# Performance work log

Hardware: AMD Instinct MI355X
Metric: run time of the kernel (lower is better)

Reference implementation:

```python
import jax, jax.numpy as jnp
import numpy as np

V, E, H, TAGS = 50000, 128, 128, 8  # H = hidden per direction (hidden_dim // 2)
B, T = 64, 512


def _lstm_dir(x, w_ih, w_hh, b_ih, b_hh, reverse):
    # x: [B,T,I] -> hs: [B,T,H]; PyTorch gate order i,f,g,o
    xg = jnp.einsum('bti,gi->btg', x, w_ih) + b_ih + b_hh  # [B,T,4H]
    if reverse:
        xg = xg[:, ::-1]
    Bn = x.shape[0]
    Hn = w_hh.shape[1]

    def step(carry, g):
        h, c = carry
        g = g + h @ w_hh.T
        i, f, gg, o = jnp.split(g, 4, axis=-1)
        c = jax.nn.sigmoid(f) * c + jax.nn.sigmoid(i) * jnp.tanh(gg)
        h = jax.nn.sigmoid(o) * jnp.tanh(c)
        return (h, c), h

    h0 = jnp.zeros((Bn, Hn), x.dtype)
    _, hs = jax.lax.scan(step, (h0, h0), jnp.swapaxes(xg, 0, 1))
    hs = jnp.swapaxes(hs, 0, 1)
    return hs[:, ::-1] if reverse else hs


def _crf_partition(emissions, transitions):
    # emissions: [B,T,K]; scan the forward algorithm over time
    fv0 = emissions[:, 0]  # [B,K]

    def step(fv, emit):
        fv = jax.nn.logsumexp(fv[:, :, None] + transitions[None] + emit[:, None, :], axis=1)
        return fv, None

    fv, _ = jax.lax.scan(step, fv0, jnp.swapaxes(emissions[:, 1:], 0, 1))
    return jax.nn.logsumexp(fv, axis=1)  # [B]


def _forward_nll(sentences, tags, embedding, lstm_params, h2t_w, h2t_b, transitions):
    x = embedding[sentences]  # [B,T,E]; dropout inactive (eval)
    for pf, pb in lstm_params:
        x = jnp.concatenate([_lstm_dir(x, *pf, False), _lstm_dir(x, *pb, True)], axis=-1)
    emissions = x @ h2t_w.T + h2t_b  # [B,T,K]
    # gold path score (mask = all ones)
    emit_score = jnp.take_along_axis(emissions, tags[:, :, None], axis=2)[..., 0].sum(axis=1)
    trans_score = transitions[tags[:, :-1], tags[:, 1:]].sum(axis=1)
    partition = _crf_partition(emissions, transitions)
    return -(emit_score + trans_score - partition).mean()


def setup_inputs() -> dict:
    key = jax.random.key(0)
    ks = jax.random.split(key, 40)
    sc = 0.05
    inp = {}
    inp['sentences'] = jax.random.randint(ks[0], (B, T), 0, V)
    inp['tags'] = jax.random.randint(ks[1], (B, T), 0, TAGS)
    emb = jax.random.normal(ks[2], (V, E), jnp.float32) * sc
    inp['embedding'] = emb.at[0].set(0.0)  # padding_idx=0
    idx = 3
    for l in range(2):
        in_dim = E if l == 0 else 2 * H
        for d in ('', '_rev'):
            inp[f'w_ih_l{l}{d}'] = jax.random.normal(ks[idx], (4 * H, in_dim), jnp.float32) * sc; idx += 1
            inp[f'w_hh_l{l}{d}'] = jax.random.normal(ks[idx], (4 * H, H), jnp.float32) * sc; idx += 1
            inp[f'b_ih_l{l}{d}'] = jax.random.normal(ks[idx], (4 * H,), jnp.float32) * sc; idx += 1
            inp[f'b_hh_l{l}{d}'] = jax.random.normal(ks[idx], (4 * H,), jnp.float32) * sc; idx += 1
    inp['h2t_w'] = jax.random.normal(ks[idx], (TAGS, 2 * H), jnp.float32) * sc; idx += 1
    inp['h2t_b'] = jax.random.normal(ks[idx], (TAGS,), jnp.float32) * sc; idx += 1
    trans = jax.random.normal(ks[idx], (TAGS, TAGS), jnp.float32)
    inp['transitions'] = trans.at[0, :].set(-10000.0).at[:, 0].set(-10000.0)
    return inp


def reference(sentences, tags, embedding,
              w_ih_l0, w_hh_l0, b_ih_l0, b_hh_l0,
              w_ih_l0_rev, w_hh_l0_rev, b_ih_l0_rev, b_hh_l0_rev,
              w_ih_l1, w_hh_l1, b_ih_l1, b_hh_l1,
              w_ih_l1_rev, w_hh_l1_rev, b_ih_l1_rev, b_hh_l1_rev,
              h2t_w, h2t_b, transitions):
    lstm_params = [
        ((w_ih_l0, w_hh_l0, b_ih_l0, b_hh_l0), (w_ih_l0_rev, w_hh_l0_rev, b_ih_l0_rev, b_hh_l0_rev)),
        ((w_ih_l1, w_hh_l1, b_ih_l1, b_hh_l1), (w_ih_l1_rev, w_hh_l1_rev, b_ih_l1_rev, b_hh_l1_rev)),
    ]
    return _forward_nll(sentences, tags, embedding, lstm_params, h2t_w, h2t_b, transitions)
```

## Files before the change

### kernel.cpp

```cpp
#include <hip/hip_runtime.h>
#include <cstdint>
#include <cstddef>

typedef __attribute__((ext_vector_type(8))) short bf16x8;
typedef __attribute__((ext_vector_type(8))) int   v8i;
typedef __attribute__((ext_vector_type(4))) float f32x4;

__device__ __forceinline__ unsigned short f2bf(float x) {
    union { float f; unsigned u; } v; v.f = x;
    unsigned r = (v.u + 0x7fffu + ((v.u >> 16) & 1u)) >> 16;
    return (unsigned short)r;
}
__device__ __forceinline__ unsigned short f2bf_trunc(float x) {
    union { float f; unsigned u; } v; v.f = x;
    return (unsigned short)(v.u >> 16);
}
__device__ __forceinline__ float bflo(unsigned u){ union{unsigned i;float f;}v; v.i = u << 16;        return v.f; }
__device__ __forceinline__ float bfhi(unsigned u){ union{unsigned i;float f;}v; v.i = u & 0xffff0000u; return v.f; }
__device__ __forceinline__ float frcp(float x){ return __builtin_amdgcn_rcpf(x); }
__device__ __forceinline__ float fsig(float x){ return frcp(1.f + __expf(-x)); }
__device__ __forceinline__ float ftanh(float x){ return 2.f * frcp(1.f + __expf(-2.f * x)) - 1.f; }

#define BARRIER_LGKM() asm volatile("s_waitcnt lgkmcnt(0)\n\ts_barrier" ::: "memory")

#define BB 64
#define TT 512
#define MM (BB*TT)
#define NG 1024

__device__ __forceinline__ int perm_orig(int g2) {
    return (g2 & 3) * 128 + (g2 >> 6) * 16 + ((g2 >> 4) & 3) * 4 + ((g2 >> 2) & 3);
}

__global__ void prep_kernel(
    const int* __restrict__ sentences, const float* __restrict__ emb,
    const float* __restrict__ w_ih_l0, const float* __restrict__ w_ih_l0r,
    const float* __restrict__ w_ih_l1, const float* __restrict__ w_ih_l1r,
    const float* __restrict__ w_hh_l0, const float* __restrict__ w_hh_l0r,
    const float* __restrict__ w_hh_l1, const float* __restrict__ w_hh_l1r,
    const float* __restrict__ b_ih_l0, const float* __restrict__ b_hh_l0,
    const float* __restrict__ b_ih_l0r, const float* __restrict__ b_hh_l0r,
    const float* __restrict__ b_ih_l1, const float* __restrict__ b_hh_l1,
    const float* __restrict__ b_ih_l1r, const float* __restrict__ b_hh_l1r,
    unsigned short* __restrict__ x0, unsigned short* __restrict__ W0c,
    unsigned short* __restrict__ W1c,
    int* __restrict__ Whh0q, int* __restrict__ Whh1q,
    float* __restrict__ bias0, float* __restrict__ bias1)
{
    int blk = blockIdx.x;
    if (blk < 4096) {
        int t4 = blk * 256 + threadIdx.x;
        int e4 = t4 * 4; int m = e4 >> 7; int k = e4 & 127;
        int tt = m >> 6, b = m & 63;
        int s = sentences[b * 512 + tt];
        float4 v = *(const float4*)(emb + (size_t)s * 128 + k);
        *(ushort4*)(x0 + (size_t)m * 128 + k) =
            make_ushort4(f2bf(v.x), f2bf(v.y), f2bf(v.z), f2bf(v.w));
    } else if (blk < 4224) {
        int t4 = (blk - 4096) * 256 + threadIdx.x;
        int e4 = t4 * 4; int n = e4 >> 7; int k = e4 & 127;
        int dir = n >> 9; int orig = perm_orig(n & 511);
        const float* src = dir ? w_ih_l0r : w_ih_l0;
        float4 v = *(const float4*)(src + (size_t)orig * 128 + k);
        *(ushort4*)(W0c + (size_t)n * 128 + k) =
            make_ushort4(f2bf(v.x), f2bf(v.y), f2bf(v.z), f2bf(v.w));
    } else if (blk < 4480) {
        int t4 = (blk - 4224) * 256 + threadIdx.x;
        int e4 = t4 * 4; int n = e4 >> 8; int k = e4 & 255;
        int dir = n >> 9; int orig = perm_orig(n & 511);
        const float* src = dir ? w_ih_l1r : w_ih_l1;
        float4 v = *(const float4*)(src + (size_t)orig * 256 + k);
        *(ushort4*)(W1c + (size_t)n * 256 + k) =
            make_ushort4(f2bf(v.x), f2bf(v.y), f2bf(v.z), f2bf(v.w));
    } else if (blk < 4736) {
        int lb = blk - 4480;
        int layer = lb >> 7;
        int t4 = (lb & 127) * 256 + threadIdx.x;
        int f  = t4 * 4;
        int j0   = f & 31;
        int lp   = (f >> 5) & 63;
        int quad = lp >> 4, r = lp & 15;
        int tb   = f >> 11;
        int tile = tb & 3, w = (tb >> 2) & 7, dir = tb >> 5;
        int g2 = w * 64 + tile * 16 + r;
        int orig = perm_orig(g2);
        const float* src = layer ? (dir ? w_hh_l1r : w_hh_l1)
                                 : (dir ? w_hh_l0r : w_hh_l0);
        int k = quad * 32 + j0;
        float4 v = *(const float4*)(src + (size_t)orig * 128 + k);
        int p = __builtin_amdgcn_cvt_pk_fp8_f32(v.x * 64.f, v.y * 64.f, 0, false);
        p = __builtin_amdgcn_cvt_pk_fp8_f32(v.z * 64.f, v.w * 64.f, p, true);
        (layer ? Whh1q : Whh0q)[f >> 2] = p;
    } else {
        int t = (blk - 4736) * 256 + threadIdx.x;
        int n = t & 1023;
        int dir = n >> 9; int orig = perm_orig(n & 511);
        if (t < 1024)
            bias0[n] = dir ? (b_ih_l0r[orig] + b_hh_l0r[orig]) : (b_ih_l0[orig] + b_hh_l0[orig]);
        else
            bias1[n] = dir ? (b_ih_l1r[orig] + b_hh_l1r[orig]) : (b_ih_l1[orig] + b_hh_l1[orig]);
    }
}

__global__ __launch_bounds__(256, 2) void gemm_xg(
    const unsigned short* __restrict__ W,
    const unsigned short* __restrict__ X,
    const float* __restrict__ bias,
    unsigned short* __restrict__ xgS,
    int K)
{
    __shared__ unsigned short sW[128 * 32];
    __shared__ unsigned short sX[128 * 32];
    const int tid  = threadIdx.x;
    const int lane = tid & 63;
    const int wid  = tid >> 6;
    const int w_n  = wid & 1, w_m = wid >> 1;
    const int r16  = lane & 15, quad = lane >> 4;
    const int nTile = blockIdx.x * 128;
    const int mTile = blockIdx.y * 128;

    f32x4 zero = {0.f, 0.f, 0.f, 0.f};
    f32x4 acc[4][4];
    #pragma unroll
    for (int i = 0; i < 4; ++i)
        #pragma unroll
        for (int j = 0; j < 4; ++j) acc[i][j] = zero;

    const int q0 = tid, q1 = tid + 256;
    const int r0 = q0 >> 2, c0 = q0 & 3, ko0 = c0 * 8;
    const int r1 = q1 >> 2, c1 = q1 & 3, ko1 = c1 * 8;
    const int s0 = (r0 << 2) | (c0 ^ ((r0 >> 1) & 3));
    const int s1 = (r1 << 2) | (c1 ^ ((r1 >> 1) & 3));
    const int rsw = quad ^ ((r16 >> 1) & 3);

    const unsigned short* Wp0 = W + (size_t)(nTile + r0) * K + ko0;
    const unsigned short* Wp1 = W + (size_t)(nTile + r1) * K + ko1;
    const unsigned short* Xp0 = X + (size_t)(mTile + r0) * K + ko0;
    const unsigned short* Xp1 = X + (size_t)(mTile + r1) * K + ko1;

    uint4 wv0 = *(const uint4*)(Wp0);
    uint4 wv1 = *(const uint4*)(Wp1);
    uint4 xv0 = *(const uint4*)(Xp0);
    uint4 xv1 = *(const uint4*)(Xp1);

    for (int k0 = 0; k0 < K; k0 += 32) {
        BARRIER_LGKM();
        ((uint4*)sW)[s0] = wv0;
        ((uint4*)sW)[s1] = wv1;
        ((uint4*)sX)[s0] = xv0;
        ((uint4*)sX)[s1] = xv1;
        BARRIER_LGKM();
        if (k0 + 32 < K) {
            wv0 = *(const uint4*)(Wp0 + k0 + 32);
            wv1 = *(const uint4*)(Wp1 + k0 + 32);
            xv0 = *(const uint4*)(Xp0 + k0 + 32);
            xv1 = *(const uint4*)(Xp1 + k0 + 32);
        }
        const bf16x8* sWv = (const bf16x8*)sW;
        const bf16x8* sXv = (const bf16x8*)sX;
        bf16x8 a[4], bx[4];
        #pragma unroll
        for (int i = 0; i < 4; ++i) {
            a[i]  = sWv[((w_n * 64 + i * 16 + r16) << 2) | rsw];
            bx[i] = sXv[((w_m * 64 + i * 16 + r16) << 2) | rsw];
        }
        #pragma unroll
        for (int i = 0; i < 4; ++i)
            #pragma unroll
            for (int j = 0; j < 4; ++j)
                acc[i][j] = __builtin_amdgcn_mfma_f32_16x16x32_bf16(a[i], bx[j], acc[i][j], 0, 0, 0);
    }

    const int w_idx = ((nTile & 511) >> 6) + w_n;
    const int dirn  = nTile >> 9;
    float4 bv[4];
    #pragma unroll
    for (int i = 0; i < 4; ++i)
        bv[i] = *(const float4*)(bias + nTile + w_n * 64 + i * 16 + quad * 4);
    const int t  = (mTile >> 6) + w_m;
    const size_t pbase = (size_t)(t >> 1) * 131072 + (size_t)dirn * 65536
                       + (size_t)w_idx * 512 + (size_t)(t & 1) * 4;
    #pragma unroll
    for (int j = 0; j < 4; ++j) {
        int b = j * 16 + r16;
        size_t base = pbase + (size_t)(b >> 2) * 4096;
        #pragma unroll
        for (int i = 0; i < 4; ++i) {
            f32x4 v = acc[i][j];
            ushort4 o = make_ushort4(f2bf(v.x + bv[i].x), f2bf(v.y + bv[i].y),
                                     f2bf(v.z + bv[i].z), f2bf(v.w + bv[i].w));
            *(uint2*)(xgS + base + (size_t)(quad * 16 + i * 4 + (b & 3)) * 8) = *(uint2*)&o;
        }
    }
}

__global__ __launch_bounds__(512, 1) void lstm_scan_mfma(
    const unsigned short* __restrict__ xgS,
    const unsigned char* __restrict__ whh_q,
    unsigned short* __restrict__ xnext)
{
    const int dir = blockIdx.x >> 4;
    const int bg  = blockIdx.x & 15;
    const int tid = threadIdx.x;
    const int w   = tid >> 6;
    const int lane= tid & 63;
    const int q   = lane >> 4;
    const int bl  = lane & 15;
    const int d   = bl >> 2;
    const int b4  = bl & 3;
    const int u   = w * 16 + d * 4 + q;
    const int b   = bg * 4 + b4;

    v8i afrag[4];
    {
        const unsigned char* wb = whh_q + (size_t)dir * 65536 + (size_t)w * 8192 + lane * 32;
        #pragma unroll
        for (int tile = 0; tile < 4; ++tile) {
            uint4 a0 = *(const uint4*)(wb + tile * 2048);
            uint4 a1 = *(const uint4*)(wb + tile * 2048 + 16);
            v8i av; av[0]=a0.x; av[1]=a0.y; av[2]=a0.z; av[3]=a0.w;
                    av[4]=a1.x; av[5]=a1.y; av[6]=a1.z; av[7]=a1.w;
            afrag[tile] = av;
        }
    }

    __shared__ __align__(16) unsigned char hbuf[2][576];
    if (tid < 144) ((unsigned*)hbuf[1])[tid] = 0;

    const f32x4 zero4 = {0.f, 0.f, 0.f, 0.f};

    float c = 0.f;
    const int pstep = dir ? -131072 : 131072;
    const unsigned short* xp = xgS + (size_t)(dir ? 255 : 0) * 131072
                             + (size_t)dir * 65536 + bg * 4096 + w * 512 + lane * 8;
    const int hstep = dir ? -16384 : 16384;
    unsigned short* hp = xnext + (size_t)(dir ? 511 : 0) * 16384 + b * 256 + dir * 128 + u;

    const int hw  = b4 * 144 + u;
    const int hr  = b4 * 144 + q * 32;

    auto step_body = [&](uint2 xv, const unsigned char* rb, unsigned char* wbuf) {
        uint4 h0 = *(const uint4*)(rb + hr);
        uint4 h1 = *(const uint4*)(rb + hr + 16);
        v8i bfr; bfr[0]=h0.x; bfr[1]=h0.y; bfr[2]=h0.z; bfr[3]=h0.w;
                 bfr[4]=h1.x; bfr[5]=h1.y; bfr[6]=h1.z; bfr[7]=h1.w;
        f32x4 a0 = __builtin_amdgcn_mfma_scale_f32_16x16x128_f8f6f4(afrag[0], bfr, zero4, 0, 0,
                       0, 0x79797979, 0, 0x7B7B7B7B);
        f32x4 a1 = __builtin_amdgcn_mfma_scale_f32_16x16x128_f8f6f4(afrag[1], bfr, zero4, 0, 0,
                       0, 0x79797979, 0, 0x7B7B7B7B);
        f32x4 a2 = __builtin_amdgcn_mfma_scale_f32_16x16x128_f8f6f4(afrag[2], bfr, zero4, 0, 0,
                       0, 0x79797979, 0, 0x7B7B7B7B);
        f32x4 a3 = __builtin_amdgcn_mfma_scale_f32_16x16x128_f8f6f4(afrag[3], bfr, zero4, 0, 0,
                       0, 0x79797979, 0, 0x7B7B7B7B);
        f32x4 sel = a0;
        sel = (d == 1) ? a1 : sel;
        sel = (d == 2) ? a2 : sel;
        sel = (d == 3) ? a3 : sel;
        float iv = sel.x + bflo(xv.x);
        float fv = sel.y + bfhi(xv.x);
        float gg = sel.z + bflo(xv.y);
        float ov = sel.w + bfhi(xv.y);
        float si = fsig(iv);
        float sf = fsig(fv);
        float tg = ftanh(gg);
        float so = fsig(ov);
        c = sf * c + si * tg;
        float h = so * ftanh(c);
        *hp = f2bf_trunc(h);
        hp += hstep;
        int q8 = __builtin_amdgcn_cvt_pk_fp8_f32(h * 16.f, h * 16.f, 0, false);
        wbuf[hw] = (unsigned char)(q8 & 0xff);
        BARRIER_LGKM();
    };

    uint4 ring[4];
    #pragma unroll
    for (int i = 0; i < 4; ++i)
        ring[i] = *(const uint4*)(xp + i * pstep);

    BARRIER_LGKM();

    for (int it2 = 0; it2 < 64; ++it2) {
        #pragma unroll
        for (int pp = 0; pp < 4; ++pp) {
            uint4 rv = ring[pp];
            uint2 xa, xb;
            if (dir) { xa.x = rv.z; xa.y = rv.w; xb.x = rv.x; xb.y = rv.y; }
            else     { xa.x = rv.x; xa.y = rv.y; xb.x = rv.z; xb.y = rv.w; }
            ring[pp] = *(const uint4*)(xp + 4 * pstep);
            xp += pstep;
            step_body(xa, hbuf[1], hbuf[0]);
            step_body(xb, hbuf[0], hbuf[1]);
        }
    }
}

__global__ void emis_kernel(const unsigned short* __restrict__ x2,
                            const float* __restrict__ h2t_w,
                            const float* __restrict__ h2t_b,
                            float* __restrict__ emis)
{
    int idx = blockIdx.x * 256 + threadIdx.x;
    int m = idx >> 3, tag = idx & 7;
    const unsigned short* xr = x2 + (size_t)m * 256;
    const float* wr = h2t_w + (size_t)tag * 256;
    float a0 = 0.f, a1 = 0.f, a2 = 0.f, a3 = 0.f;
    #pragma unroll 4
    for (int k = 0; k < 256; k += 8) {
        uint4 xv = *(const uint4*)(xr + k);
        float4 w0 = *(const float4*)(wr + k);
        float4 w1 = *(const float4*)(wr + k + 4);
        a0 += bflo(xv.x) * w0.x + bfhi(xv.x) * w0.y;
        a1 += bflo(xv.y) * w0.z + bfhi(xv.y) * w0.w;
        a2 += bflo(xv.z) * w1.x + bfhi(xv.z) * w1.y;
        a3 += bflo(xv.w) * w1.z + bfhi(xv.w) * w1.w;
    }
    emis[idx] = h2t_b[tag] + ((a0 + a1) + (a2 + a3));
}

__global__ void crf_chunk(const float* __restrict__ emis,
                          const float* __restrict__ trans,
                          float* __restrict__ Pc)
{
    const int b = blockIdx.x >> 3;
    const int cch = blockIdx.x & 7;
    const int l = threadIdx.x;
    const int i = l >> 3, j = l & 7;
    const int i8 = i * 8;
    float T[8];
    #pragma unroll
    for (int k = 0; k < 8; ++k) T[k] = trans[k * 8 + j];

    const int t0 = (cch == 0) ? 1 : cch * 64;
    const int t1 = cch * 64 + 64;
    const float* ej = emis + (size_t)b * 8 + j;

    float P = trans[i * 8 + j] + ej[(size_t)t0 * 512];
    float e1 = ej[(size_t)(t0 + 1) * 512];
    for (int t = t0 + 1; t < t1; ++t) {
        float v0 = __shfl(P, i8 + 0) + T[0];
        float v1 = __shfl(P, i8 + 1) + T[1];
        float v2 = __shfl(P, i8 + 2) + T[2];
        float v3 = __shfl(P, i8 + 3) + T[3];
        float v4 = __shfl(P, i8 + 4) + T[4];
        float v5 = __shfl(P, i8 + 5) + T[5];
        float v6 = __shfl(P, i8 + 6) + T[6];
        float v7 = __shfl(P, i8 + 7) + T[7];
        float m = fmaxf(fmaxf(fmaxf(v0, v1), fmaxf(v2, v3)),
                        fmaxf(fmaxf(v4, v5), fmaxf(v6, v7)));
        float s = __expf(v0 - m) + __expf(v1 - m) + __expf(v2 - m) + __expf(v3 - m)
                + __expf(v4 - m) + __expf(v5 - m) + __expf(v6 - m) + __expf(v7 - m);
        P = m + __logf(s) + e1;
        e1 = ej[(size_t)(t + 1) * 512];
    }
    Pc[((size_t)b * 8 + cch) * 64 + l] = P;
}

__global__ void crf_combine(const float* __restrict__ emis,
                            const float* __restrict__ Pc,
                            const int* __restrict__ tags,
                            const float* __restrict__ trans,
                            float* __restrict__ partials)
{
    const int l = threadIdx.x;
    const int sl = l >> 3, j = l & 7, sl8 = sl * 8;
    const int b = blockIdx.x * 8 + sl;

    float fv = emis[(size_t)b * 8 + j];
    #pragma unroll
    for (int cch = 0; cch < 8; ++cch) {
        const float* Pb = Pc + ((size_t)b * 8 + cch) * 64 + j;
        float p0 = Pb[0],  p1 = Pb[8],  p2 = Pb[16], p3 = Pb[24];
        float p4 = Pb[32], p5 = Pb[40], p6 = Pb[48], p7 = Pb[56];
        float v0 = __shfl(fv, sl8 + 0) + p0;
        float v1 = __shfl(fv, sl8 + 1) + p1;
        float v2 = __shfl(fv, sl8 + 2) + p2;
        float v3 = __shfl(fv, sl8 + 3) + p3;
        float v4 = __shfl(fv, sl8 + 4) + p4;
        float v5 = __shfl(fv, sl8 + 5) + p5;
        float v6 = __shfl(fv, sl8 + 6) + p6;
        float v7 = __shfl(fv, sl8 + 7) + p7;
        float m = fmaxf(fmaxf(fmaxf(v0, v1), fmaxf(v2, v3)),
                        fmaxf(fmaxf(v4, v5), fmaxf(v6, v7)));
        float s = __expf(v0 - m) + __expf(v1 - m) + __expf(v2 - m) + __expf(v3 - m)
                + __expf(v4 - m) + __expf(v5 - m) + __expf(v6 - m) + __expf(v7 - m);
        fv = m + __logf(s);
    }

    float m2 = fv;
    m2 = fmaxf(m2, __shfl_xor(m2, 1));
    m2 = fmaxf(m2, __shfl_xor(m2, 2));
    m2 = fmaxf(m2, __shfl_xor(m2, 4));
    float e2s = __expf(fv - m2);
    e2s += __shfl_xor(e2s, 1);
    e2s += __shfl_xor(e2s, 2);
    e2s += __shfl_xor(e2s, 4);
    float partition = m2 + __logf(e2s);

    const int* tg = tags + (size_t)b * TT;
    float sc = 0.f;
    for (int tt = j; tt < TT; tt += 8) {
        int tag = tg[tt];
        sc += emis[((size_t)tt * 64 + b) * 8 + tag];
        if (tt > 0) sc += trans[tg[tt - 1] * 8 + tag];
    }
    sc += __shfl_xor(sc, 1);
    sc += __shfl_xor(sc, 2);
    sc += __shfl_xor(sc, 4);
    if (j == 0) partials[b] = sc - partition;
}

__global__ void final_kernel(const float* __restrict__ partials, float* __restrict__ out)
{
    int l = threadIdx.x;
    float v = partials[l];
    #pragma unroll
    for (int d = 1; d < 64; d <<= 1) v += __shfl_xor(v, d);
    if (l == 0) out[0] = -v / 64.f;
}

extern "C" void kernel_launch(void* const* d_in, const int* in_sizes, int n_in,
                              void* d_out, int out_size, void* d_ws, size_t ws_size,
                              hipStream_t stream)
{
    const int*   sentences = (const int*)d_in[0];
    const int*   tags      = (const int*)d_in[1];
    const float* embedding = (const float*)d_in[2];
    const float* w_ih_l0   = (const float*)d_in[3];
    const float* w_hh_l0   = (const float*)d_in[4];
    const float* b_ih_l0   = (const float*)d_in[5];
    const float* b_hh_l0   = (const float*)d_in[6];
    const float* w_ih_l0r  = (const float*)d_in[7];
    const float* w_hh_l0r  = (const float*)d_in[8];
    const float* b_ih_l0r  = (const float*)d_in[9];
    const float* b_hh_l0r  = (const float*)d_in[10];
    const float* w_ih_l1   = (const float*)d_in[11];
    const float* w_hh_l1   = (const float*)d_in[12];
    const float* b_ih_l1   = (const float*)d_in[13];
    const float* b_hh_l1   = (const float*)d_in[14];
    const float* w_ih_l1r  = (const float*)d_in[15];
    const float* w_hh_l1r  = (const float*)d_in[16];
    const float* b_ih_l1r  = (const float*)d_in[17];
    const float* b_hh_l1r  = (const float*)d_in[18];
    const float* h2t_w     = (const float*)d_in[19];
    const float* h2t_b     = (const float*)d_in[20];
    const float* trans     = (const float*)d_in[21];

    char* ws = (char*)d_ws;
    unsigned short* W0c   = (unsigned short*)(ws + 0);
    unsigned short* W1c   = (unsigned short*)(ws + 262144);
    int*  Whh0q           = (int*)(ws + 786432);
    int*  Whh1q           = (int*)(ws + 917504);
    float* bias0          = (float*)(ws + 1310720);
    float* bias1          = (float*)(ws + 1314816);
    float* emis           = (float*)(ws + 1318912);
    float* partials       = (float*)(ws + 2375680);
    float* Pc             = (float*)(ws + 2375936);
    unsigned short* xgS   = (unsigned short*)(ws + 4194304);
    unsigned short* x0    = (unsigned short*)(ws + 71303168);
    unsigned short* x1    = (unsigned short*)(ws + 72351744);
    unsigned short* x2    = x1;
    (void)ws_size; (void)in_sizes; (void)n_in; (void)out_size;

    prep_kernel<<<4744, 256, 0, stream>>>(sentences, embedding,
        w_ih_l0, w_ih_l0r, w_ih_l1, w_ih_l1r,
        w_hh_l0, w_hh_l0r, w_hh_l1, w_hh_l1r,
        b_ih_l0, b_hh_l0, b_ih_l0r, b_hh_l0r,
        b_ih_l1, b_hh_l1, b_ih_l1r, b_hh_l1r,
        x0, W0c, W1c, Whh0q, Whh1q, bias0, bias1);

    gemm_xg<<<dim3(8, 256), 256, 0, stream>>>(W0c, x0, bias0, xgS, 128);
    lstm_scan_mfma<<<32, 512, 0, stream>>>(xgS, (const unsigned char*)Whh0q, x1);
    gemm_xg<<<dim3(8, 256), 256, 0, stream>>>(W1c, x1, bias1, xgS, 256);
    lstm_scan_mfma<<<32, 512, 0, stream>>>(xgS, (const unsigned char*)Whh1q, x2);
    emis_kernel<<<1024, 256, 0, stream>>>(x2, h2t_w, h2t_b, emis);
    crf_chunk<<<512, 64, 0, stream>>>(emis, trans, Pc);
    crf_combine<<<8, 64, 0, stream>>>(emis, Pc, tags, trans, partials);
    final_kernel<<<1, 64, 0, stream>>>(partials, (float*)d_out);
}
```

Measured before the change: 645.5 us.

## Fold log2e scaling into LSTM weights and gates, repack xg layout, fuse final reduction

The recurrent weights and the xg gate pre-activations are pre-scaled by -log2(e) (and -2·log2(e) for the cell gate), so the scan can use exp2 directly instead of exp with a negation. The xg store layout is reorganised so the GEMM writes 16-byte vectors and each scan lane loads two 8-byte halves, with 32-bit offset arithmetic. The final reduction kernel is removed: crf_combine reduces within its wave and atomically adds into a zeroed output. Together these cut per-step ALU work in the serial scan and drop one launch, at the cost of fp32 atomics, which make the summation order nondeterministic.

```diff
diff --git a/kernel.cpp b/kernel.cpp
--- a/kernel.cpp
+++ b/kernel.cpp
@@ -18,8 +18,6 @@
 __device__ __forceinline__ float bflo(unsigned u){ union{unsigned i;float f;}v; v.i = u << 16;        return v.f; }
 __device__ __forceinline__ float bfhi(unsigned u){ union{unsigned i;float f;}v; v.i = u & 0xffff0000u; return v.f; }
 __device__ __forceinline__ float frcp(float x){ return __builtin_amdgcn_rcpf(x); }
-__device__ __forceinline__ float fsig(float x){ return frcp(1.f + __expf(-x)); }
-__device__ __forceinline__ float ftanh(float x){ return 2.f * frcp(1.f + __expf(-2.f * x)) - 1.f; }
 
 #define BARRIER_LGKM() asm volatile("s_waitcnt lgkmcnt(0)\n\ts_barrier" ::: "memory")
 
@@ -27,6 +25,9 @@
 #define TT 512
 #define MM (BB*TT)
 #define NG 1024
+
+#define NL2E  -1.442695f
+#define N2L2E -2.885390f
 
 __device__ __forceinline__ int perm_orig(int g2) {
     return (g2 & 3) * 128 + (g2 >> 6) * 16 + ((g2 >> 4) & 3) * 4 + ((g2 >> 2) & 3);
@@ -87,9 +88,10 @@
         const float* src = layer ? (dir ? w_hh_l1r : w_hh_l1)
                                  : (dir ? w_hh_l0r : w_hh_l0);
         int k = quad * 32 + j0;
+        float fac = ((r & 3) == 2) ? (N2L2E * 64.f) : (NL2E * 64.f);
         float4 v = *(const float4*)(src + (size_t)orig * 128 + k);
-        int p = __builtin_amdgcn_cvt_pk_fp8_f32(v.x * 64.f, v.y * 64.f, 0, false);
-        p = __builtin_amdgcn_cvt_pk_fp8_f32(v.z * 64.f, v.w * 64.f, p, true);
+        int p = __builtin_amdgcn_cvt_pk_fp8_f32(v.x * fac, v.y * fac, 0, false);
+        p = __builtin_amdgcn_cvt_pk_fp8_f32(v.z * fac, v.w * fac, p, true);
         (layer ? Whh1q : Whh0q)[f >> 2] = p;
     } else {
         int t = (blk - 4736) * 256 + threadIdx.x;
@@ -178,19 +180,29 @@
     for (int i = 0; i < 4; ++i)
         bv[i] = *(const float4*)(bias + nTile + w_n * 64 + i * 16 + quad * 4);
     const int t  = (mTile >> 6) + w_m;
-    const size_t pbase = (size_t)(t >> 1) * 131072 + (size_t)dirn * 65536
-                       + (size_t)w_idx * 512 + (size_t)(t & 1) * 4;
+    const unsigned pb = (unsigned)(t >> 1) * 131072u + (unsigned)dirn * 65536u
+                      + (unsigned)w_idx * 512u + (unsigned)(t & 1) * 256u
+                      + (unsigned)quad * 64u;
     #pragma unroll
     for (int j = 0; j < 4; ++j) {
         int b = j * 16 + r16;
-        size_t base = pbase + (size_t)(b >> 2) * 4096;
+        unsigned base = pb + (unsigned)(b >> 2) * 4096u + (unsigned)(b & 3) * 16u;
+        ushort4 o[4];
         #pragma unroll
         for (int i = 0; i < 4; ++i) {
             f32x4 v = acc[i][j];
-            ushort4 o = make_ushort4(f2bf(v.x + bv[i].x), f2bf(v.y + bv[i].y),
-                                     f2bf(v.z + bv[i].z), f2bf(v.w + bv[i].w));
-            *(uint2*)(xgS + base + (size_t)(quad * 16 + i * 4 + (b & 3)) * 8) = *(uint2*)&o;
+            o[i] = make_ushort4(f2bf((v.x + bv[i].x) * NL2E),
+                                f2bf((v.y + bv[i].y) * NL2E),
+                                f2bf((v.z + bv[i].z) * N2L2E),
+                                f2bf((v.w + bv[i].w) * NL2E));
         }
+        uint4 pk0, pk1;
+        pk0.x = *(unsigned*)&o[0].x; pk0.y = *((unsigned*)&o[0].x + 1);
+        pk0.z = *(unsigned*)&o[1].x; pk0.w = *((unsigned*)&o[1].x + 1);
+        pk1.x = *(unsigned*)&o[2].x; pk1.y = *((unsigned*)&o[2].x + 1);
+        pk1.z = *(unsigned*)&o[3].x; pk1.w = *((unsigned*)&o[3].x + 1);
+        *(uint4*)(xgS + base)     = pk0;
+        *(uint4*)(xgS + base + 8) = pk1;
     }
 }
 
@@ -205,9 +217,8 @@
     const int w   = tid >> 6;
     const int lane= tid & 63;
     const int q   = lane >> 4;
-    const int bl  = lane & 15;
-    const int d   = bl >> 2;
-    const int b4  = bl & 3;
+    const int b4  = (lane >> 2) & 3;
+    const int d   = lane & 3;
     const int u   = w * 16 + d * 4 + q;
     const int b   = bg * 4 + b4;
 
@@ -230,11 +241,16 @@
     const f32x4 zero4 = {0.f, 0.f, 0.f, 0.f};
 
     float c = 0.f;
+    const unsigned short* xb_ptr = xgS + dir * 65536 + bg * 4096 - 524288;
+    unsigned xoff = 524288u + (dir ? 255u * 131072u : 0u)
+                  + (unsigned)w * 512u + (unsigned)lane * 4u;
     const int pstep = dir ? -131072 : 131072;
-    const unsigned short* xp = xgS + (size_t)(dir ? 255 : 0) * 131072
-                             + (size_t)dir * 65536 + bg * 4096 + w * 512 + lane * 8;
+    const unsigned tha = dir ? 256u : 0u;
+    const unsigned thb = dir ? 0u : 256u;
+
+    unsigned short* hb_ptr = xnext + dir * 128;
+    unsigned hoff = (dir ? 511u * 16384u : 0u) + (unsigned)b * 256u + (unsigned)u;
     const int hstep = dir ? -16384 : 16384;
-    unsigned short* hp = xnext + (size_t)(dir ? 511 : 0) * 16384 + b * 256 + dir * 128 + u;
 
     const int hw  = b4 * 144 + u;
     const int hr  = b4 * 144 + q * 32;
@@ -260,35 +276,37 @@
         float fv = sel.y + bfhi(xv.x);
         float gg = sel.z + bflo(xv.y);
         float ov = sel.w + bfhi(xv.y);
-        float si = fsig(iv);
-        float sf = fsig(fv);
-        float tg = ftanh(gg);
-        float so = fsig(ov);
+        float si = frcp(1.f + exp2f(iv));
+        float sf = frcp(1.f + exp2f(fv));
+        float so = frcp(1.f + exp2f(ov));
+        float tg = 2.f * frcp(1.f + exp2f(gg)) - 1.f;
         c = sf * c + si * tg;
-        float h = so * ftanh(c);
-        *hp = f2bf_trunc(h);
-        hp += hstep;
+        float tc = 2.f * frcp(1.f + exp2f(N2L2E * c)) - 1.f;
+        float h = so * tc;
+        hb_ptr[hoff] = f2bf_trunc(h);
+        hoff += hstep;
         int q8 = __builtin_amdgcn_cvt_pk_fp8_f32(h * 16.f, h * 16.f, 0, false);
         wbuf[hw] = (unsigned char)(q8 & 0xff);
         BARRIER_LGKM();
     };
 
-    uint4 ring[4];
-    #pragma unroll
-    for (int i = 0; i < 4; ++i)
-        ring[i] = *(const uint4*)(xp + i * pstep);
+    uint2 ringA[4], ringB[4];
+    #pragma unroll
+    for (int i = 0; i < 4; ++i) {
+        ringA[i] = *(const uint2*)(xb_ptr + (xoff + i * pstep + tha));
+        ringB[i] = *(const uint2*)(xb_ptr + (xoff + i * pstep + thb));
+    }
 
     BARRIER_LGKM();
 
     for (int it2 = 0; it2 < 64; ++it2) {
         #pragma unroll
         for (int pp = 0; pp < 4; ++pp) {
-            uint4 rv = ring[pp];
-            uint2 xa, xb;
-            if (dir) { xa.x = rv.z; xa.y = rv.w; xb.x = rv.x; xb.y = rv.y; }
-            else     { xa.x = rv.x; xa.y = rv.y; xb.x = rv.z; xb.y = rv.w; }
-            ring[pp] = *(const uint4*)(xp + 4 * pstep);
-            xp += pstep;
+            uint2 xa = ringA[pp];
+            uint2 xb = ringB[pp];
+            ringA[pp] = *(const uint2*)(xb_ptr + (xoff + 4 * pstep + tha));
+            ringB[pp] = *(const uint2*)(xb_ptr + (xoff + 4 * pstep + thb));
+            xoff += pstep;
             step_body(xa, hbuf[1], hbuf[0]);
             step_body(xb, hbuf[0], hbuf[1]);
         }
@@ -360,7 +378,7 @@
                             const float* __restrict__ Pc,
                             const int* __restrict__ tags,
                             const float* __restrict__ trans,
-                            float* __restrict__ partials)
+                            float* __restrict__ out)
 {
     const int l = threadIdx.x;
     const int sl = l >> 3, j = l & 7, sl8 = sl * 8;
@@ -407,16 +425,11 @@
     sc += __shfl_xor(sc, 1);
     sc += __shfl_xor(sc, 2);
     sc += __shfl_xor(sc, 4);
-    if (j == 0) partials[b] = sc - partition;
-}
-
-__global__ void final_kernel(const float* __restrict__ partials, float* __restrict__ out)
-{
-    int l = threadIdx.x;
-    float v = partials[l];
-    #pragma unroll
-    for (int d = 1; d < 64; d <<= 1) v += __shfl_xor(v, d);
-    if (l == 0) out[0] = -v / 64.f;
+
+    float val = (j == 0) ? (partition - sc) * 0.015625f : 0.f;
+    #pragma unroll
+    for (int dd = 1; dd < 64; dd <<= 1) val += __shfl_xor(val, dd);
+    if (l == 0) atomicAdd(out, val);
 }
 
 extern "C" void kernel_launch(void* const* d_in, const int* in_sizes, int n_in,
@@ -454,7 +467,6 @@
     float* bias0          = (float*)(ws + 1310720);
     float* bias1          = (float*)(ws + 1314816);
     float* emis           = (float*)(ws + 1318912);
-    float* partials       = (float*)(ws + 2375680);
     float* Pc             = (float*)(ws + 2375936);
     unsigned short* xgS   = (unsigned short*)(ws + 4194304);
     unsigned short* x0    = (unsigned short*)(ws + 71303168);
@@ -462,6 +474,8 @@
     unsigned short* x2    = x1;
     (void)ws_size; (void)in_sizes; (void)n_in; (void)out_size;
 
+    hipMemsetAsync(d_out, 0, sizeof(float), stream);
+
     prep_kernel<<<4744, 256, 0, stream>>>(sentences, embedding,
         w_ih_l0, w_ih_l0r, w_ih_l1, w_ih_l1r,
         w_hh_l0, w_hh_l0r, w_hh_l1, w_hh_l1r,
@@ -475,6 +489,5 @@
     lstm_scan_mfma<<<32, 512, 0, stream>>>(xgS, (const unsigned char*)Whh1q, x2);
     emis_kernel<<<1024, 256, 0, stream>>>(x2, h2t_w, h2t_b, emis);
     crf_chunk<<<512, 64, 0, stream>>>(emis, trans, Pc);
-    crf_combine<<<8, 64, 0, stream>>>(emis, Pc, tags, trans, partials);
-    final_kernel<<<1, 64, 0, stream>>>(partials, (float*)d_out);
-}
+    crf_combine<<<8, 64, 0, stream>>>(emis, Pc, tags, trans, (float*)d_out);
+}
```

Result: slower. 710.4 us (+10.1%).
